# Performance work log

Measured on AMD Instinct MI355X. Metric: run time of the kernel, lower is better.

## Reference

```python
import jax, jax.numpy as jnp
import numpy as np

B, N, D, K = 4, 8192, 128, 32
LN_EPS = 1e-5


def setup_inputs() -> dict:
    key = jax.random.key(0)
    k1, k2, k3, k4 = jax.random.split(key, 4)
    x = jax.random.normal(k1, (B, N, D), dtype=jnp.float32)
    adj = jax.random.randint(k2, (B, N, K), 0, N, dtype=jnp.int64)
    W = jax.random.normal(k3, (2 * D, D), dtype=jnp.float32) * (1.0 / np.sqrt(2 * D))
    b = jnp.zeros((D,), dtype=jnp.float32)
    gamma = jnp.ones((D,), dtype=jnp.float32)
    beta = jnp.zeros((D,), dtype=jnp.float32)
    return {"x": x, "adj": adj, "W": W, "b": b, "gamma": gamma, "beta": beta}


def reference(x, adj, W, b, gamma, beta):
    # Gather neighbor features: neigh[b,n,k,:] = x[b, adj[b,n,k], :]
    # (avoids the original's (B,N,N,D) blowup; direct index gather)
    neigh = jnp.take_along_axis(x[:, None, :, :], adj[..., None], axis=2)  # (B,N,K,D)
    neigh_mean = neigh.mean(axis=2)  # (B,N,D)
    h = jnp.concatenate([x, neigh_mean], axis=-1)  # (B,N,2D)
    h = jnp.einsum('bnf,fd->bnd', h, W) + b
    h = jax.nn.gelu(h, approximate=False)
    # dropout is identity in eval mode
    y = h + x
    mu = y.mean(axis=-1, keepdims=True)
    var = y.var(axis=-1, keepdims=True)
    return (y - mu) * jax.lax.rsqrt(var + LN_EPS) * gamma + beta
```

## Files before the change

kernel.cpp:

```cpp
#include <hip/hip_runtime.h>

#define B_ 4
#define N_ 8192
#define D_ 128
#define K_ 32

typedef short short8 __attribute__((ext_vector_type(8)));
typedef float f32x4 __attribute__((ext_vector_type(4)));

__device__ __forceinline__ unsigned short f2bf(float f) {
  unsigned int u = __float_as_uint(f);
  u += 0x7FFFu + ((u >> 16) & 1u);
  return (unsigned short)(u >> 16);
}
__device__ __forceinline__ float bf2f(unsigned short h) {
  return __uint_as_float(((unsigned int)h) << 16);
}

__global__ __launch_bounds__(256) void cvt_w_kernel(const float* __restrict__ W,
                                                    unsigned short* __restrict__ Wt) {
  int e = blockIdx.x * 256 + threadIdx.x;
  int d = e & 127, fglob = e >> 7;
  int is_v = fglob >> 7, floc = fglob & 127;
  Wt[(is_v * 128 + d) * 128 + floc] = f2bf(W[e]);
}

__global__ __launch_bounds__(512) void gemm_kernel(
    const float* __restrict__ x, const unsigned short* __restrict__ Wt,
    unsigned short* __restrict__ P) {
  __shared__ __align__(16) unsigned char in_tile[64 * 256];

  const int t = threadIdx.x, wave = t >> 6, lane = t & 63;
  const int l15 = lane & 15, kg = lane >> 4;
  const long row0 = (long)blockIdx.x * 64;

  #pragma unroll
  for (int i = 0; i < 4; ++i) {
    int idx = t + i * 512;
    int row = idx >> 5, cs = idx & 31;
    float4 v = *reinterpret_cast<const float4*>(x + (row0 + row) * D_ + cs * 4);
    ushort4 o;
    o.x = f2bf(v.x); o.y = f2bf(v.y); o.z = f2bf(v.z); o.w = f2bf(v.w);
    *reinterpret_cast<ushort4*>(
        in_tile + ((row * 256 + cs * 8) ^ ((row & 7) << 4))) = o;
  }

  const int halfw = wave & 3, is_v = wave >> 2;
  short8 bw[2][4];
  #pragma unroll
  for (int tt = 0; tt < 2; ++tt) {
    const int col = is_v * 128 + halfw * 32 + tt * 16 + l15;
    #pragma unroll
    for (int ks = 0; ks < 4; ++ks)
      bw[tt][ks] = *reinterpret_cast<const short8*>(
          Wt + col * 128 + ks * 32 + kg * 8);
  }
  __syncthreads();

  f32x4 acc[4][2];
  #pragma unroll
  for (int r = 0; r < 4; ++r)
    #pragma unroll
    for (int tt = 0; tt < 2; ++tt)
      acc[r][tt] = (f32x4){0.f, 0.f, 0.f, 0.f};

  #pragma unroll
  for (int ks = 0; ks < 4; ++ks) {
    #pragma unroll
    for (int r = 0; r < 4; ++r) {
      int row = r * 16 + l15;
      short8 af = *reinterpret_cast<const short8*>(
          in_tile + ((row * 256 + ks * 64 + kg * 16) ^ ((row & 7) << 4)));
      acc[r][0] = __builtin_amdgcn_mfma_f32_16x16x32_bf16(af, bw[0][ks], acc[r][0], 0, 0, 0);
      acc[r][1] = __builtin_amdgcn_mfma_f32_16x16x32_bf16(af, bw[1][ks], acc[r][1], 0, 0, 0);
    }
  }

  #pragma unroll
  for (int r = 0; r < 4; ++r)
    #pragma unroll
    for (int tt = 0; tt < 2; ++tt) {
      const int col = is_v * 128 + halfw * 32 + tt * 16 + l15;
      #pragma unroll
      for (int i = 0; i < 4; ++i) {
        int row = r * 16 + kg * 4 + i;
        P[(row0 + row) * 256 + col] = f2bf(acc[r][tt][i]);
      }
    }
}

__global__ __launch_bounds__(256) void gather_kernel(
    const int* __restrict__ adj, const unsigned short* __restrict__ P,
    const float* __restrict__ x, const float* __restrict__ bias,
    const float* __restrict__ gamma, const float* __restrict__ beta,
    float* __restrict__ out) {
  const int t = threadIdx.x;
  const int wave = t >> 6, lane = t & 63;
  const int vblk = ((blockIdx.x & 7) << 8) + (blockIdx.x >> 3);
  const int node_base = vblk * 16 + wave * 4;
  const int b = node_base >> 13;
  const unsigned int* pd = (const unsigned int*)P;
  const unsigned int* vbase = pd + ((size_t)b << 13) * 128 + 64 + lane;
  const int c0 = lane * 2;
  const float2 bi = *reinterpret_cast<const float2*>(bias + c0);
  const float2 ga = *reinterpret_cast<const float2*>(gamma + c0);
  const float2 be = *reinterpret_cast<const float2*>(beta + c0);
  const int nbu = __builtin_amdgcn_readfirstlane(node_base);

  #pragma unroll
  for (int j = 0; j < 4; ++j) {
    const int gn = nbu + j;
    const int* ap = adj + (size_t)gn * K_;
    float a0 = 0.f, a1 = 0.f;
    #pragma unroll
    for (int k = 0; k < K_; ++k) {
      unsigned int v = vbase[(size_t)ap[k] * 128];
      a0 += __uint_as_float(v << 16);
      a1 += __uint_as_float(v & 0xFFFF0000u);
    }
    const unsigned int ud = pd[(size_t)gn * 128 + lane];
    const float2 xv = *reinterpret_cast<const float2*>(x + (size_t)gn * D_ + c0);
    float h0 = __uint_as_float(ud << 16)        + a0 * 0.03125f + bi.x;
    float h1 = __uint_as_float(ud & 0xFFFF0000u) + a1 * 0.03125f + bi.y;
    h0 = 0.5f * h0 * (1.f + erff(h0 * 0.70710678118f));
    h1 = 0.5f * h1 * (1.f + erff(h1 * 0.70710678118f));
    const float y0 = h0 + xv.x, y1 = h1 + xv.y;
    float s = y0 + y1, sq = y0 * y0 + y1 * y1;
    #pragma unroll
    for (int off = 1; off < 64; off <<= 1) {
      s  += __shfl_xor(s, off, 64);
      sq += __shfl_xor(sq, off, 64);
    }
    const float mu   = s * (1.f / 128.f);
    const float rstd = rsqrtf(sq * (1.f / 128.f) - mu * mu + 1e-5f);
    float2 o;
    o.x = (y0 - mu) * rstd * ga.x + be.x;
    o.y = (y1 - mu) * rstd * ga.y + be.y;
    *reinterpret_cast<float2*>(out + (size_t)gn * D_ + c0) = o;
  }
}

__global__ __launch_bounds__(512) void fused_f32_kernel(
    const float* __restrict__ x, const int* __restrict__ adj,
    const float* __restrict__ W, const float* __restrict__ bias,
    const float* __restrict__ gamma, const float* __restrict__ beta,
    float* __restrict__ out) {
  __shared__ __align__(16) unsigned char smem[40960];
  unsigned char* in_tile = smem;
  int* adj_lds = (int*)(smem + 32768);
  float* y = (float*)smem;
  const int t = threadIdx.x, wave = t >> 6, lane = t & 63;
  const int l15 = lane & 15, kg = lane >> 4;
  const int vid = (blockIdx.x & 7) * 64 + (blockIdx.x >> 3);
  const int bidx = vid >> 7;
  const long row0 = (long)bidx * N_ + (vid & 127) * 64;
  #pragma unroll
  for (int i = 0; i < 4; ++i)
    adj_lds[t + i * 512] = adj[row0 * K_ + t + i * 512];
  #pragma unroll
  for (int i = 0; i < 4; ++i) {
    int idx = t + i * 512;
    int row = idx >> 5, cp = (idx & 31) * 4;
    float4 v = *reinterpret_cast<const float4*>(x + (row0 + row) * D_ + cp);
    ushort4 o;
    o.x = f2bf(v.x); o.y = f2bf(v.y); o.z = f2bf(v.z); o.w = f2bf(v.w);
    *reinterpret_cast<ushort4*>(in_tile + row * 512 + ((2 * cp) ^ ((row & 7) << 4))) = o;
  }
  __syncthreads();
  {
    const int g = t & 31, rb = t >> 5, c0 = g * 4;
    #pragma unroll
    for (int batch = 0; batch < 4; ++batch) {
      int row = rb + batch * 16;
      const int* ap = adj_lds + row * K_;
      float a0 = 0, a1 = 0, a2 = 0, a3 = 0;
      for (int k = 0; k < K_; ++k) {
        float4 v = *reinterpret_cast<const float4*>(x + ((long)bidx * N_ + ap[k]) * D_ + c0);
        a0 += v.x; a1 += v.y; a2 += v.z; a3 += v.w;
      }
      ushort4 m;
      m.x = f2bf(a0 * 0.03125f); m.y = f2bf(a1 * 0.03125f);
      m.z = f2bf(a2 * 0.03125f); m.w = f2bf(a3 * 0.03125f);
      *reinterpret_cast<ushort4*>(in_tile + row * 512 +
                                  ((2 * (D_ + c0)) ^ ((row & 7) << 4))) = m;
    }
  }
  __syncthreads();
  const int dl = (wave << 4) + l15;
  f32x4 acc[4];
  #pragma unroll
  for (int r = 0; r < 4; ++r) acc[r] = (f32x4){0.f, 0.f, 0.f, 0.f};
  #pragma unroll
  for (int ks = 0; ks < 8; ++ks) {
    short8 bwk;
    #pragma unroll
    for (int j = 0; j < 8; ++j)
      bwk[j] = (short)f2bf(W[(ks * 32 + kg * 8 + j) * D_ + dl]);
    #pragma unroll
    for (int r = 0; r < 4; ++r) {
      int row = r * 16 + l15;
      short8 af = *reinterpret_cast<const short8*>(
          in_tile + row * 512 + ((2 * (ks * 32 + kg * 8)) ^ ((row & 7) << 4)));
      acc[r] = __builtin_amdgcn_mfma_f32_16x16x32_bf16(af, bwk, acc[r], 0, 0, 0);
    }
  }
  __syncthreads();
  const float bv = bias[dl];
  #pragma unroll
  for (int r = 0; r < 4; ++r)
    #pragma unroll
    for (int i = 0; i < 4; ++i) {
      int row = r * 16 + kg * 4 + i;
      float h = acc[r][i] + bv;
      float ge = 0.5f * h * (1.f + erff(h * 0.70710678118f));
      y[row * 132 + dl] = ge + x[(row0 + row) * D_ + dl];
    }
  __syncthreads();
  {
    const int row = t >> 3, l8 = t & 7;
    const float* yr = y + row * 132 + l8 * 16;
    float4 v[4];
    float s = 0.f, sq = 0.f;
    #pragma unroll
    for (int i = 0; i < 4; ++i) {
      v[i] = *reinterpret_cast<const float4*>(yr + i * 4);
      s += v[i].x + v[i].y + v[i].z + v[i].w;
      sq += v[i].x * v[i].x + v[i].y * v[i].y + v[i].z * v[i].z + v[i].w * v[i].w;
    }
    #pragma unroll
    for (int off = 1; off < 8; off <<= 1) {
      s += __shfl_xor(s, off, 64);
      sq += __shfl_xor(sq, off, 64);
    }
    const float mu = s * (1.f / 128.f);
    const float rstd = rsqrtf(sq * (1.f / 128.f) - mu * mu + 1e-5f);
    float* orow = out + (row0 + row) * D_ + l8 * 16;
    #pragma unroll
    for (int i = 0; i < 4; ++i) {
      float4 g = *reinterpret_cast<const float4*>(gamma + l8 * 16 + i * 4);
      float4 bb = *reinterpret_cast<const float4*>(beta + l8 * 16 + i * 4);
      float4 o;
      o.x = (v[i].x - mu) * rstd * g.x + bb.x;
      o.y = (v[i].y - mu) * rstd * g.y + bb.y;
      o.z = (v[i].z - mu) * rstd * g.z + bb.z;
      o.w = (v[i].w - mu) * rstd * g.w + bb.w;
      *reinterpret_cast<float4*>(orow + i * 4) = o;
    }
  }
}

extern "C" void kernel_launch(void* const* d_in, const int* in_sizes, int n_in,
                              void* d_out, int out_size, void* d_ws, size_t ws_size,
                              hipStream_t stream) {
  const float* x     = (const float*)d_in[0];
  const int*   adj   = (const int*)d_in[1];
  const float* W     = (const float*)d_in[2];
  const float* bias  = (const float*)d_in[3];
  const float* gamma = (const float*)d_in[4];
  const float* beta  = (const float*)d_in[5];
  float* out = (float*)d_out;

  const size_t p_bytes  = (size_t)B_ * N_ * 256 * 2;
  const size_t wt_bytes = (size_t)256 * 128 * 2;

  if (ws_size >= p_bytes + wt_bytes) {
    unsigned short* P  = (unsigned short*)d_ws;
    unsigned short* Wt = (unsigned short*)((char*)d_ws + p_bytes);
    cvt_w_kernel<<<dim3(128), dim3(256), 0, stream>>>(W, Wt);
    gemm_kernel<<<dim3((B_ * N_) / 64), dim3(512), 0, stream>>>(x, Wt, P);
    gather_kernel<<<dim3(2048), dim3(256), 0, stream>>>(
        adj, P, x, bias, gamma, beta, out);
  } else {
    fused_f32_kernel<<<dim3((B_ * N_) / 64), dim3(512), 0, stream>>>(
        x, adj, W, bias, gamma, beta, out);
  }
}
```

Baseline: 108.4 us.

## Stage GEMM output through LDS and process two nodes per wave in gather

The GEMM epilogue now writes bf16 results into a swizzled shared-memory tile and then stores them to global memory as 16-byte vectors, replacing scattered 2-byte stores. The gather kernel splits each wave into two 32-lane halves that handle two nodes at once. Each lane covers 4 columns with 8-byte loads, and neighbor indices are loaded once per wave and broadcast with shuffles instead of per-lane scalar adj loads. This is meant to widen memory transactions and raise memory-level parallelism, at the cost of 32KB of extra LDS in the GEMM, which may reduce occupancy there.

```diff
diff --git a/kernel.cpp b/kernel.cpp
--- a/kernel.cpp
+++ b/kernel.cpp
@@ -29,6 +29,7 @@
     const float* __restrict__ x, const unsigned short* __restrict__ Wt,
     unsigned short* __restrict__ P) {
   __shared__ __align__(16) unsigned char in_tile[64 * 256];
+  __shared__ __align__(16) unsigned char out_tile[64 * 512];
 
   const int t = threadIdx.x, wave = t >> 6, lane = t & 63;
   const int l15 = lane & 15, kg = lane >> 4;
@@ -84,9 +85,21 @@
       #pragma unroll
       for (int i = 0; i < 4; ++i) {
         int row = r * 16 + kg * 4 + i;
-        P[(row0 + row) * 256 + col] = f2bf(acc[r][tt][i]);
+        *reinterpret_cast<unsigned short*>(
+            out_tile + ((row * 512 + col * 2) ^ ((row & 7) << 4))) =
+            f2bf(acc[r][tt][i]);
       }
     }
+  __syncthreads();
+
+  #pragma unroll
+  for (int p = 0; p < 4; ++p) {
+    int idx = t + p * 512;
+    int row = idx >> 5, cb = (idx & 31) * 16;
+    uint4 v = *reinterpret_cast<const uint4*>(
+        out_tile + ((row * 512 + cb) ^ ((row & 7) << 4)));
+    *reinterpret_cast<uint4*>(P + (row0 + row) * 256 + (cb >> 1)) = v;
+  }
 }
 
 __global__ __launch_bounds__(256) void gather_kernel(
@@ -96,47 +109,56 @@
     float* __restrict__ out) {
   const int t = threadIdx.x;
   const int wave = t >> 6, lane = t & 63;
+  const int l31 = lane & 31, hs = lane & 32;
   const int vblk = ((blockIdx.x & 7) << 8) + (blockIdx.x >> 3);
-  const int node_base = vblk * 16 + wave * 4;
-  const int b = node_base >> 13;
+  const int nb0 = vblk * 16 + wave * 4;
+  const int b = nb0 >> 13;
   const unsigned int* pd = (const unsigned int*)P;
-  const unsigned int* vbase = pd + ((size_t)b << 13) * 128 + 64 + lane;
-  const int c0 = lane * 2;
-  const float2 bi = *reinterpret_cast<const float2*>(bias + c0);
-  const float2 ga = *reinterpret_cast<const float2*>(gamma + c0);
-  const float2 be = *reinterpret_cast<const float2*>(beta + c0);
-  const int nbu = __builtin_amdgcn_readfirstlane(node_base);
-
-  #pragma unroll
-  for (int j = 0; j < 4; ++j) {
-    const int gn = nbu + j;
-    const int* ap = adj + (size_t)gn * K_;
-    float a0 = 0.f, a1 = 0.f;
+  const unsigned int* vb_dw = pd + (size_t)b * N_ * 128 + 64 + l31 * 2;
+  const int c0 = l31 * 4;
+  const float4 bi = *reinterpret_cast<const float4*>(bias + c0);
+  const float4 ga = *reinterpret_cast<const float4*>(gamma + c0);
+  const float4 be = *reinterpret_cast<const float4*>(beta + c0);
+
+  #pragma unroll
+  for (int j = 0; j < 2; ++j) {
+    const int nb = nb0 + j * 2;
+    const int gn = nb + (lane >> 5);
+    const int av = adj[(size_t)nb * K_ + lane];
+    float a0 = 0.f, a1 = 0.f, a2 = 0.f, a3 = 0.f;
     #pragma unroll
     for (int k = 0; k < K_; ++k) {
-      unsigned int v = vbase[(size_t)ap[k] * 128];
-      a0 += __uint_as_float(v << 16);
-      a1 += __uint_as_float(v & 0xFFFF0000u);
-    }
-    const unsigned int ud = pd[(size_t)gn * 128 + lane];
-    const float2 xv = *reinterpret_cast<const float2*>(x + (size_t)gn * D_ + c0);
-    float h0 = __uint_as_float(ud << 16)        + a0 * 0.03125f + bi.x;
-    float h1 = __uint_as_float(ud & 0xFFFF0000u) + a1 * 0.03125f + bi.y;
+      int rowk = __shfl(av, hs | k, 64);
+      ushort4 v = *reinterpret_cast<const ushort4*>(vb_dw + (size_t)rowk * 128);
+      a0 += bf2f(v.x); a1 += bf2f(v.y); a2 += bf2f(v.z); a3 += bf2f(v.w);
+    }
+    const ushort4 ud = *reinterpret_cast<const ushort4*>(pd + (size_t)gn * 128 + l31 * 2);
+    const float4 xv = *reinterpret_cast<const float4*>(x + (size_t)gn * D_ + c0);
+    float h0 = bf2f(ud.x) + a0 * 0.03125f + bi.x;
+    float h1 = bf2f(ud.y) + a1 * 0.03125f + bi.y;
+    float h2 = bf2f(ud.z) + a2 * 0.03125f + bi.z;
+    float h3 = bf2f(ud.w) + a3 * 0.03125f + bi.w;
     h0 = 0.5f * h0 * (1.f + erff(h0 * 0.70710678118f));
     h1 = 0.5f * h1 * (1.f + erff(h1 * 0.70710678118f));
+    h2 = 0.5f * h2 * (1.f + erff(h2 * 0.70710678118f));
+    h3 = 0.5f * h3 * (1.f + erff(h3 * 0.70710678118f));
     const float y0 = h0 + xv.x, y1 = h1 + xv.y;
-    float s = y0 + y1, sq = y0 * y0 + y1 * y1;
-    #pragma unroll
-    for (int off = 1; off < 64; off <<= 1) {
+    const float y2 = h2 + xv.z, y3 = h3 + xv.w;
+    float s = y0 + y1 + y2 + y3;
+    float sq = y0 * y0 + y1 * y1 + y2 * y2 + y3 * y3;
+    #pragma unroll
+    for (int off = 1; off < 32; off <<= 1) {
       s  += __shfl_xor(s, off, 64);
       sq += __shfl_xor(sq, off, 64);
     }
     const float mu   = s * (1.f / 128.f);
     const float rstd = rsqrtf(sq * (1.f / 128.f) - mu * mu + 1e-5f);
-    float2 o;
+    float4 o;
     o.x = (y0 - mu) * rstd * ga.x + be.x;
     o.y = (y1 - mu) * rstd * ga.y + be.y;
-    *reinterpret_cast<float2*>(out + (size_t)gn * D_ + c0) = o;
+    o.z = (y2 - mu) * rstd * ga.z + be.z;
+    o.w = (y3 - mu) * rstd * ga.w + be.w;
+    *reinterpret_cast<float4*>(out + (size_t)gn * D_ + c0) = o;
   }
 }
 
```

New measurement: 108.3 us. Within noise of the previous version (-0.1%).
